# Kernel tuning notes

Hardware: AMD Instinct MI355X
Metric: run time of the kernel (lower is better)

The kernel has to match this reference:

```python
import jax, jax.numpy as jnp
import numpy as np
from jax import lax

MAX_OBJ = 100
IOU_THRES = 0.45
SCORE_THRES = 0.25
MAX_WH = 7680.0

# xywh -> xyxy conversion matrix (same as ONNX_ORT.convert_matrix)
CONVERT = jnp.array([[1, 0, 1, 0],
                     [0, 1, 0, 1],
                     [-0.5, 0, 0.5, 0],
                     [0, -0.5, 0, 0.5]], dtype=jnp.float32)


def _iou_one_vs_all(box, boxes):
    # box: [4] xyxy, boxes: [N,4] xyxy
    x1 = jnp.maximum(box[0], boxes[:, 0])
    y1 = jnp.maximum(box[1], boxes[:, 1])
    x2 = jnp.minimum(box[2], boxes[:, 2])
    y2 = jnp.minimum(box[3], boxes[:, 3])
    inter = jnp.clip(x2 - x1, 0.0) * jnp.clip(y2 - y1, 0.0)
    a = (box[2] - box[0]) * (box[3] - box[1])
    b = (boxes[:, 2] - boxes[:, 0]) * (boxes[:, 3] - boxes[:, 1])
    return inter / (a + b - inter + 1e-9)


def _nms_indices(nmsbox, max_score):
    # Greedy class-offset NMS; returns [MAX_OBJ] indices, -1 for padding.
    valid0 = max_score >= SCORE_THRES

    def step(valid, _):
        s = jnp.where(valid, max_score, -1.0)
        i = jnp.argmax(s)
        ok = s[i] >= SCORE_THRES
        iou = _iou_one_vs_all(nmsbox[i], nmsbox)
        valid = valid & (iou <= IOU_THRES)
        valid = valid.at[i].set(False)
        return valid, jnp.where(ok, i, -1)

    _, idxs = lax.scan(step, valid0, None, length=MAX_OBJ)
    return idxs


def _forward(x1, x2, num_labels1, num_labels2):
    B, N1, _ = x1.shape
    N2 = x2.shape[1]
    # pad x1 class scores with zeros for model2's labels (appended at end)
    x1p = jnp.concatenate([x1, jnp.zeros((B, N1, num_labels2), x1.dtype)], axis=2)
    # pad x2: insert zeros for model1's labels between conf and its own classes
    x2p = jnp.concatenate([x2[:, :, 0:5],
                           jnp.zeros((B, N2, num_labels1), x2.dtype),
                           x2[:, :, 5:]], axis=2)
    x = jnp.concatenate([x1p, x2p], axis=1)  # [B, N1+N2, 5+C1+C2]

    boxes = x[:, :, :4] @ CONVERT            # xywh -> xyxy, [B,N,4]
    conf = x[:, :, 4:5]
    scores = x[:, :, 5:] * conf              # [B,N,C]
    max_score = scores.max(axis=2)           # [B,N]
    cat_id = scores.argmax(axis=2)           # [B,N]
    # class-offset boxes so NMS is class-aware
    nmsbox = boxes + cat_id[..., None].astype(boxes.dtype) * MAX_WH

    idxs = jax.vmap(_nms_indices)(lax.stop_gradient(nmsbox),
                                  lax.stop_gradient(max_score))  # [B,MAX_OBJ]
    mask = idxs >= 0
    si = jnp.maximum(idxs, 0)
    sel_boxes = jnp.take_along_axis(boxes, si[..., None], axis=1)      # [B,MAX_OBJ,4]
    sel_cat = jnp.take_along_axis(cat_id, si, axis=1).astype(boxes.dtype)
    sel_score = jnp.take_along_axis(max_score, si, axis=1)

    mf = mask.astype(boxes.dtype)
    Xcol = jnp.where(mask, jnp.arange(B)[:, None], -1).astype(boxes.dtype)
    out = jnp.concatenate([Xcol[..., None],
                           sel_boxes * mf[..., None],
                           (sel_cat * mf)[..., None],
                           (sel_score * mf)[..., None]], axis=2)
    return out.reshape(B * MAX_OBJ, 7)


def setup_inputs() -> dict:
    key = jax.random.key(0)
    k1, k2 = jax.random.split(key)
    x1 = jax.random.uniform(k1, (4, 25200, 85), dtype=jnp.float32)
    x2 = jax.random.uniform(k2, (4, 25200, 25), dtype=jnp.float32)
    return {"x1": x1, "x2": x2, "num_labels1": 80, "num_labels2": 20}


def reference(x1, x2, num_labels1, num_labels2):
    return _forward(x1, x2, num_labels1, num_labels2)
```

## Files before the change

kernel.cpp:

```cpp
#include <hip/hip_runtime.h>
#include <stdint.h>

#pragma clang fp contract(off)

#define BATCH 4
#define N1 25200
#define NROW 50400
#define NCLS 100
#define TOT (BATCH*NROW)
#define CAPB 1280
#define SCORE_T 0.25f
#define IOU_T 0.45f
#define MAXWH 7680.0f

#define X1_SLAB 64
#define X1_SPB 394
#define X2_SLAB 256
#define X2_SPB 99

#define BIN_SLICES 128
#define BIN_SL 394

typedef unsigned long long u64;

__device__ __forceinline__ u64 pack_key(unsigned sb, int n, int cid) {
    return ((u64)sb << 32) | ((u64)(unsigned)((n ^ 0xFFFF) & 0xFFFF) << 8) | (u64)(unsigned)cid;
}

__device__ __forceinline__ bool sup_test(float inter, float sum) {
    float d = (sum - inter) + 1e-9f;
    float t1 = IOU_T * d;
    bool hi = inter > t1 * 1.00001f;
    bool lo = inter < t1 * 0.99999f;
    if (__builtin_expect(!(hi || lo), 0)) return (inter / d) > IOU_T;
    return hi;
}

__device__ __forceinline__ float rl(float v, int srcLane) {
    return __int_as_float(__builtin_amdgcn_readlane(__float_as_int(v), srcLane));
}

__device__ __forceinline__ void blk2bucket(int blk, int& b, int& c) {
    if (blk < BATCH * 20) { b = blk / 20; c = 80 + (blk - b * 20); }
    else { int z = blk - BATCH * 20; b = z / 80; c = z - b * 80; }
}

__device__ __forceinline__ int prefix_ge(const u64* list, int cnt, u64 T) {
    int lo = 0, hi = cnt;
    while (lo < hi) {
        int mid = (lo + hi) >> 1;
        if (list[mid] >= T) lo = mid + 1; else hi = mid;
    }
    return lo;
}

__device__ __forceinline__ void sort_desc(u64* sk, int L, int t) {
    bool act = (t * 8) < L;
    u64 r[8];
    if (act) {
#pragma unroll
        for (int e = 0; e < 8; ++e) r[e] = sk[t * 8 + e];
    }
    for (int k = 2; k <= L; k <<= 1) {
        for (int j = k >> 1; j > 0; j >>= 1) {
            if (j >= 512) {
                if (act) {
#pragma unroll
                    for (int e = 0; e < 8; ++e) sk[t * 8 + e] = r[e];
                }
                __syncthreads();
                if (act) {
                    bool iAmLo = (t & (j >> 3)) == 0;
                    bool descSeg = (t & (k >> 3)) == 0;
                    bool takeMax = (descSeg == iAmLo);
#pragma unroll
                    for (int e = 0; e < 8; ++e) {
                        u64 u = r[e];
                        u64 v = sk[(t * 8 + e) ^ j];
                        bool uGE = (u >= v);
                        r[e] = (takeMax == uGE) ? u : v;
                    }
                }
                __syncthreads();
            } else if (j >= 8) {
                if (act) {
                    int dt = j >> 3;
                    bool iAmLo = (t & dt) == 0;
                    bool descSeg = (t & (k >> 3)) == 0;
                    bool takeMax = (descSeg == iAmLo);
#pragma unroll
                    for (int e = 0; e < 8; ++e) {
                        u64 u = r[e];
                        u64 v = __shfl_xor(u, dt, 64);
                        bool uGE = (u >= v);
                        r[e] = (takeMax == uGE) ? u : v;
                    }
                }
            } else {
                if (act) {
#pragma unroll
                    for (int e = 0; e < 8; ++e) {
                        if (!(e & j)) {
                            int e2 = e | j;
                            bool descSeg = (k >= 8) ? ((t & (k >> 3)) == 0)
                                                    : ((e & k) == 0);
                            u64 lo = r[e], hi = r[e2];
                            bool sw = descSeg ? (lo < hi) : (lo > hi);
                            if (sw) { r[e] = hi; r[e2] = lo; }
                        }
                    }
                }
            }
        }
    }
    if (act) {
#pragma unroll
        for (int e = 0; e < 8; ++e) sk[t * 8 + e] = r[e];
    }
    __syncthreads();
}

__global__ __launch_bounds__(256) void k_rows(const float* __restrict__ x1,
                                              const float* __restrict__ x2,
                                              float4* __restrict__ boxes4,
                                              u64* __restrict__ rowKey) {
    __shared__ float4 ld4[1600];
    float* ld = (float*)ld4;
    int blk = blockIdx.x;
    int t = threadIdx.x;
    const int NX1 = BATCH * X1_SPB;
    if (blk < NX1) {
        int b = blk / X1_SPB, s = blk - b * X1_SPB;
        int r0 = s * X1_SLAB;
        int nr = min(X1_SLAB, N1 - r0);
        const float4* src = (const float4*)(x1 + ((size_t)b * N1 + r0) * 85);
        int count4 = (nr * 85) >> 2;
        for (int i = t; i < count4; i += 256) ld4[i] = src[i];
        __syncthreads();
        int row = t >> 2, sub = t & 3;
        if (row < nr) {
            const float* p = ld + row * 85;
            float conf = p[4];
            u64 key = 0ULL;
            int base = sub * 20;
            for (int c = 0; c < 20; ++c) {
                int j = base + c;
                float v = p[5 + j] * conf;
                u64 kk = ((u64)__float_as_uint(v) << 32) | (unsigned)~(unsigned)j;
                if (kk > key) key = kk;
            }
            u64 o;
            o = __shfl_xor(key, 1, 64); if (o > key) key = o;
            o = __shfl_xor(key, 2, 64); if (o > key) key = o;
            if (sub == 0) {
                float best = __uint_as_float((unsigned)(key >> 32));
                int bestj = ~(unsigned)key;
                int n = r0 + row;
                int r = b * NROW + n;
                u64 outk = 0ULL;
                if (best >= SCORE_T) {
                    float cx = p[0], cy = p[1], w = p[2], h = p[3];
                    boxes4[r] = make_float4(cx - 0.5f * w, cy - 0.5f * h,
                                            cx + 0.5f * w, cy + 0.5f * h);
                    outk = pack_key((unsigned)(key >> 32), n, bestj);
                }
                rowKey[r] = outk;
            }
        }
    } else {
        int blk2 = blk - NX1;
        int b = blk2 / X2_SPB, s = blk2 - b * X2_SPB;
        int r0 = s * X2_SLAB;
        int nr = min(X2_SLAB, N1 - r0);
        const float4* src = (const float4*)(x2 + ((size_t)b * N1 + r0) * 25);
        int count4 = (nr * 25) >> 2;
        for (int i = t; i < count4; i += 256) ld4[i] = src[i];
        __syncthreads();
        if (t < nr) {
            const float* p = ld + t * 25;
            float conf = p[4];
            float best = 0.0f; int bestj = 0;
            for (int j2 = 0; j2 < 20; ++j2) {
                float v = p[5 + j2] * conf;
                if (v > best) { best = v; bestj = 80 + j2; }
            }
            int n = N1 + r0 + t;
            int r = b * NROW + n;
            u64 outk = 0ULL;
            if (best >= SCORE_T) {
                float cx = p[0], cy = p[1], w = p[2], h = p[3];
                boxes4[r] = make_float4(cx - 0.5f * w, cy - 0.5f * h,
                                        cx + 0.5f * w, cy + 0.5f * h);
                outk = pack_key(__float_as_uint(best), n, bestj);
            }
            rowKey[r] = outk;
        }
    }
}

__global__ __launch_bounds__(256) void k_bin(const u64* __restrict__ rowKey,
                                             u64* __restrict__ csrKey,
                                             int* __restrict__ fill) {
    __shared__ u64 keys[BIN_SL];
    __shared__ int cnt[NCLS];
    __shared__ int base[NCLS];
    __shared__ int cur[NCLS];
    int blk = blockIdx.x;
    int b = blk / BIN_SLICES, s = blk - b * BIN_SLICES;
    int r0 = s * BIN_SL;
    int nr = min(BIN_SL, NROW - r0);
    int t = threadIdx.x;
    if (t < NCLS) { cnt[t] = 0; cur[t] = 0; }
    __syncthreads();
    const u64* src = rowKey + (size_t)b * NROW + r0;
    for (int i = t; i < nr; i += 256) {
        u64 k = src[i];
        keys[i] = k;
        if (k != 0ULL) atomicAdd(&cnt[(int)(k & 0xFF)], 1);
    }
    __syncthreads();
    if (t < NCLS && cnt[t] > 0)
        base[t] = atomicAdd(&fill[b * NCLS + t], cnt[t]);
    __syncthreads();
    for (int i = t; i < nr; i += 256) {
        u64 k = keys[i];
        if (k != 0ULL) {
            int c = (int)(k & 0xFF);
            int p = base[c] + atomicAdd(&cur[c], 1);
            if (p < CAPB) csrKey[(size_t)(b * NCLS + c) * CAPB + p] = k;
        }
    }
}

__global__ __launch_bounds__(256) void k_nms(const float4* __restrict__ boxes4,
                                             const u64* __restrict__ csrKey,
                                             const int* __restrict__ fill,
                                             u64* __restrict__ accKey,
                                             int* __restrict__ accCnt) {
    __shared__ u64 sk[2048];
    __shared__ float4 cQ[CAPB];
    __shared__ float4 accQ[100];
    __shared__ float accA[100];
    int b, c; blk2bucket(blockIdx.x, b, c);
    int bucket = b * NCLS + c;
    int t = threadIdx.x;
    int lane = t & 63;
    int cnt0 = min(fill[bucket], CAPB);
    if (cnt0 == 0) { if (t == 0) accCnt[bucket] = 0; return; }
    const u64* src = csrKey + (size_t)bucket * CAPB;
    int L = 512; while (L < cnt0) L <<= 1;
    for (int i = t; i < L; i += 256) sk[i] = (i < cnt0) ? src[i] : 0ULL;
    __syncthreads();
    sort_desc(sk, L, t);
    float off = (float)c * MAXWH;
    for (int i = t; i < cnt0; i += 256) {
        u64 k = sk[i];
        int n = 0xFFFF ^ (int)((k >> 8) & 0xFFFF);
        float4 v = boxes4[b * NROW + n];
        v.x += off; v.y += off; v.z += off; v.w += off;
        cQ[i] = v;
    }
    __syncthreads();
    if (t >= 64) return;

    int m = 0;
    for (int base = 0; base < cnt0 && m < 100; base += 64) {
        int j = base + lane;
        bool alive = (j < cnt0);
        float4 a = make_float4(0.f, 0.f, 0.f, 0.f);
        float aA = 0.f; u64 myKey = 0ULL;
        if (alive) {
            myKey = sk[j];
            a = cQ[j];
            aA = (a.z - a.x) * (a.w - a.y);
        }
        int k2 = 0;
        while (k2 < m) {
            if (__ballot(alive) == 0ULL) break;
            int rem = m - k2;
            if (rem >= 8) {
#pragma unroll
                for (int u = 0; u < 8; ++u) {
                    float4 q = accQ[k2 + u];
                    float qa = accA[k2 + u];
                    float xx1 = fmaxf(a.x, q.x), yy1 = fmaxf(a.y, q.y);
                    float xx2 = fminf(a.z, q.z), yy2 = fminf(a.w, q.w);
                    float inter = fmaxf(xx2 - xx1, 0.f) * fmaxf(yy2 - yy1, 0.f);
                    alive = alive && !sup_test(inter, qa + aA);
                }
                k2 += 8;
            } else {
                for (int u = 0; u < rem; ++u) {
                    float4 q = accQ[k2 + u];
                    float qa = accA[k2 + u];
                    float xx1 = fmaxf(a.x, q.x), yy1 = fmaxf(a.y, q.y);
                    float xx2 = fminf(a.z, q.z), yy2 = fminf(a.w, q.w);
                    float inter = fmaxf(xx2 - xx1, 0.f) * fmaxf(yy2 - yy1, 0.f);
                    alive = alive && !sup_test(inter, qa + aA);
                }
                k2 = m;
            }
        }
        u64 av = __ballot(alive);
        int accIdx = -1;
        while (av != 0ULL && m < 100) {
            int f = __builtin_ctzll(av);
            float qx = rl(a.x, f), qy = rl(a.y, f);
            float qz = rl(a.z, f), qw = rl(a.w, f);
            if (lane == f) { accIdx = m; alive = false; }
            ++m;
            if (alive) {
                float qa = (qz - qx) * (qw - qy);
                float xx1 = fmaxf(a.x, qx), yy1 = fmaxf(a.y, qy);
                float xx2 = fminf(a.z, qz), yy2 = fminf(a.w, qw);
                float inter = fmaxf(xx2 - xx1, 0.f) * fmaxf(yy2 - yy1, 0.f);
                alive = !sup_test(inter, qa + aA);
            }
            av = __ballot(alive);
        }
        if (accIdx >= 0) {
            accQ[accIdx] = a; accA[accIdx] = aA;
            accKey[(size_t)bucket * 100 + accIdx] = myKey;
        }
    }
    if (lane == 0) accCnt[bucket] = m;
}

__global__ __launch_bounds__(256) void k_merge(const float4* __restrict__ boxes4,
                                               const u64* __restrict__ accKey,
                                               const int* __restrict__ accCnt,
                                               float* __restrict__ out) {
    __shared__ u64 sk[1024];
    __shared__ u64 head[NCLS];
    __shared__ int cnts[NCLS];
    __shared__ int pc[NCLS];
    int b = blockIdx.x, t = threadIdx.x;
    const u64* base = accKey + (size_t)b * NCLS * 100;
    if (t < NCLS) {
        int cc = accCnt[b * NCLS + t];
        cnts[t] = cc;
        head[t] = (cc > 0) ? base[t * 100] : 0ULL;
    }
    __syncthreads();
    int S = 0, ne = 0; u64 mn = ~0ULL;
    for (int c = 0; c < NCLS; ++c) {
        int cc = cnts[c];
        S += cc;
        if (cc > 0) { ++ne; u64 h = head[c]; if (h < mn) mn = h; }
    }
    u64 T;
    bool bisect;
    if (S <= 900)            { T = 0ULL; bisect = false; }
    else if (ne == NCLS)     { T = mn;   bisect = false; }
    else                     { T = 0ULL; bisect = true;  }
    if (t < NCLS) pc[t] = bisect ? 0 : prefix_ge(base + t * 100, cnts[t], T);
    __syncthreads();
    int G = 0;
    for (int c = 0; c < NCLS; ++c) G += pc[c];
    if (G > 1000) bisect = true;
    if (bisect) {
        u64 lo = 0ULL, hi = ~0ULL;
        for (int it = 0; it < 64; ++it) {
            u64 mid = lo + ((hi - lo) >> 1);
            if (t < NCLS) pc[t] = prefix_ge(base + t * 100, cnts[t], mid);
            __syncthreads();
            int cnt = 0;
            for (int c = 0; c < NCLS; ++c) cnt += pc[c];
            if (cnt >= 100 && cnt <= 1000) { T = mid; G = cnt; break; }
            if (cnt < 100) hi = mid; else lo = mid;
            __syncthreads();
        }
    }
    if (t < NCLS) {
        int off = 0;
        for (int c = 0; c < t; ++c) off += pc[c];
        int p = pc[t];
        for (int j = 0; j < p; ++j) sk[off + j] = base[t * 100 + j];
    }
    for (int i = G + t; i < 1024; i += 256) sk[i] = 0ULL;
    __syncthreads();
    sort_desc(sk, 1024, t);
    if (t < 100) {
        u64 k = sk[t];
        float* o7 = out + (size_t)(b * 100 + t) * 7;
        if (k == 0ULL) {
            o7[0] = -1.0f;
            o7[1] = 0.0f; o7[2] = 0.0f; o7[3] = 0.0f;
            o7[4] = 0.0f; o7[5] = 0.0f; o7[6] = 0.0f;
        } else {
            int n = 0xFFFF ^ (int)((k >> 8) & 0xFFFF);
            int cid = (int)(k & 0xFF);
            float4 bx = boxes4[b * NROW + n];
            o7[0] = (float)b;
            o7[1] = bx.x; o7[2] = bx.y; o7[3] = bx.z; o7[4] = bx.w;
            o7[5] = (float)cid;
            o7[6] = __uint_as_float((unsigned)(k >> 32));
        }
    }
}

extern "C" void kernel_launch(void* const* d_in, const int* in_sizes, int n_in,
                              void* d_out, int out_size, void* d_ws, size_t ws_size,
                              hipStream_t stream) {
    const float* x1 = (const float*)d_in[0];
    const float* x2 = (const float*)d_in[1];
    float* out = (float*)d_out;

    float4* boxes4 = (float4*)d_ws;
    u64* rowKey = (u64*)(boxes4 + TOT);
    u64* csrKey = rowKey + TOT;
    u64* accKey = csrKey + (size_t)BATCH * NCLS * CAPB;
    int* fill   = (int*)(accKey + (size_t)BATCH * NCLS * 100);
    int* accCnt = fill + BATCH * NCLS;

    hipMemsetAsync(fill, 0, sizeof(int) * BATCH * NCLS, stream);

    int rowBlocks = BATCH * X1_SPB + BATCH * X2_SPB;
    k_rows<<<rowBlocks, 256, 0, stream>>>(x1, x2, boxes4, rowKey);
    k_bin<<<BATCH * BIN_SLICES, 256, 0, stream>>>(rowKey, csrKey, fill);
    k_nms<<<BATCH * NCLS, 256, 0, stream>>>(boxes4, csrKey, fill, accKey, accCnt);
    k_merge<<<BATCH, 256, 0, stream>>>(boxes4, accKey, accCnt, out);
}
```

Before: 134.3 us.

## Parallelize per-class NMS suppression across four wavefronts per block

The NMS kernel previously ran the greedy suppression on a single wavefront, leaving the other three idle. Now all four wavefronts test a 256-candidate group against the already accepted boxes in parallel and publish alive masks through shared memory. Wavefront 0 then sequentially resolves the survivors against boxes accepted within the group. This adds two block barriers per group and some redundant recomputation in exchange for more parallel IoU work.

Measured after the change: 134.5 us. No clear change (+0.1%).

```diff
diff --git a/kernel.cpp b/kernel.cpp
--- a/kernel.cpp
+++ b/kernel.cpp
@@ -241,10 +241,12 @@
     __shared__ float4 cQ[CAPB];
     __shared__ float4 accQ[100];
     __shared__ float accA[100];
+    __shared__ u64 aliveMask[4];
+    __shared__ int mSh;
     int b, c; blk2bucket(blockIdx.x, b, c);
     int bucket = b * NCLS + c;
     int t = threadIdx.x;
-    int lane = t & 63;
+    int lane = t & 63, wid = t >> 6;
     int cnt0 = min(fill[bucket], CAPB);
     if (cnt0 == 0) { if (t == 0) accCnt[bucket] = 0; return; }
     const u64* src = csrKey + (size_t)bucket * CAPB;
@@ -260,70 +262,116 @@
         v.x += off; v.y += off; v.z += off; v.w += off;
         cQ[i] = v;
     }
-    __syncthreads();
-    if (t >= 64) return;
-
-    int m = 0;
-    for (int base = 0; base < cnt0 && m < 100; base += 64) {
-        int j = base + lane;
-        bool alive = (j < cnt0);
-        float4 a = make_float4(0.f, 0.f, 0.f, 0.f);
-        float aA = 0.f; u64 myKey = 0ULL;
-        if (alive) {
-            myKey = sk[j];
-            a = cQ[j];
-            aA = (a.z - a.x) * (a.w - a.y);
-        }
-        int k2 = 0;
-        while (k2 < m) {
-            if (__ballot(alive) == 0ULL) break;
-            int rem = m - k2;
-            if (rem >= 8) {
-#pragma unroll
-                for (int u = 0; u < 8; ++u) {
-                    float4 q = accQ[k2 + u];
-                    float qa = accA[k2 + u];
-                    float xx1 = fmaxf(a.x, q.x), yy1 = fmaxf(a.y, q.y);
-                    float xx2 = fminf(a.z, q.z), yy2 = fminf(a.w, q.w);
-                    float inter = fmaxf(xx2 - xx1, 0.f) * fmaxf(yy2 - yy1, 0.f);
-                    alive = alive && !sup_test(inter, qa + aA);
-                }
-                k2 += 8;
-            } else {
-                for (int u = 0; u < rem; ++u) {
-                    float4 q = accQ[k2 + u];
-                    float qa = accA[k2 + u];
-                    float xx1 = fmaxf(a.x, q.x), yy1 = fmaxf(a.y, q.y);
-                    float xx2 = fminf(a.z, q.z), yy2 = fminf(a.w, q.w);
-                    float inter = fmaxf(xx2 - xx1, 0.f) * fmaxf(yy2 - yy1, 0.f);
-                    alive = alive && !sup_test(inter, qa + aA);
-                }
-                k2 = m;
-            }
-        }
-        u64 av = __ballot(alive);
-        int accIdx = -1;
-        while (av != 0ULL && m < 100) {
-            int f = __builtin_ctzll(av);
-            float qx = rl(a.x, f), qy = rl(a.y, f);
-            float qz = rl(a.z, f), qw = rl(a.w, f);
-            if (lane == f) { accIdx = m; alive = false; }
-            ++m;
-            if (alive) {
-                float qa = (qz - qx) * (qw - qy);
-                float xx1 = fmaxf(a.x, qx), yy1 = fmaxf(a.y, qy);
-                float xx2 = fminf(a.z, qz), yy2 = fminf(a.w, qw);
-                float inter = fmaxf(xx2 - xx1, 0.f) * fmaxf(yy2 - yy1, 0.f);
-                alive = !sup_test(inter, qa + aA);
-            }
-            av = __ballot(alive);
-        }
-        if (accIdx >= 0) {
-            accQ[accIdx] = a; accA[accIdx] = aA;
-            accKey[(size_t)bucket * 100 + accIdx] = myKey;
-        }
-    }
-    if (lane == 0) accCnt[bucket] = m;
+    if (t == 0) mSh = 0;
+    __syncthreads();
+
+    int nG = (cnt0 + 255) >> 8;
+    for (int g = 0; g < nG; ++g) {
+        int mSnap = mSh;
+        if (mSnap < 100) {
+            int j = ((g << 2) + wid) * 64 + lane;
+            bool alive = (j < cnt0);
+            float4 a = make_float4(0.f, 0.f, 0.f, 0.f);
+            float aA = 0.f;
+            if (alive) { a = cQ[j]; aA = (a.z - a.x) * (a.w - a.y); }
+            int k2 = 0;
+            while (k2 < mSnap) {
+                if (__ballot(alive) == 0ULL) break;
+                int rem = mSnap - k2;
+                if (rem >= 8) {
+#pragma unroll
+                    for (int u = 0; u < 8; ++u) {
+                        float4 q = accQ[k2 + u];
+                        float qa = accA[k2 + u];
+                        float xx1 = fmaxf(a.x, q.x), yy1 = fmaxf(a.y, q.y);
+                        float xx2 = fminf(a.z, q.z), yy2 = fminf(a.w, q.w);
+                        float inter = fmaxf(xx2 - xx1, 0.f) * fmaxf(yy2 - yy1, 0.f);
+                        alive = alive && !sup_test(inter, qa + aA);
+                    }
+                    k2 += 8;
+                } else {
+                    for (int u = 0; u < rem; ++u) {
+                        float4 q = accQ[k2 + u];
+                        float qa = accA[k2 + u];
+                        float xx1 = fmaxf(a.x, q.x), yy1 = fmaxf(a.y, q.y);
+                        float xx2 = fminf(a.z, q.z), yy2 = fminf(a.w, q.w);
+                        float inter = fmaxf(xx2 - xx1, 0.f) * fmaxf(yy2 - yy1, 0.f);
+                        alive = alive && !sup_test(inter, qa + aA);
+                    }
+                    k2 = mSnap;
+                }
+            }
+            u64 wmask = __ballot(alive);
+            if (lane == 0) aliveMask[wid] = wmask;
+        }
+        __syncthreads();
+        if (mSnap < 100 && wid == 0) {
+            int mNow = mSnap;
+            for (int s = 0; s < 4 && mNow < 100; ++s) {
+                int j = ((g << 2) + s) * 64 + lane;
+                bool alive = ((aliveMask[s] >> lane) & 1ULL) && (j < cnt0);
+                float4 a = make_float4(0.f, 0.f, 0.f, 0.f);
+                float aA = 0.f; u64 myKey = 0ULL;
+                if (alive) {
+                    a = cQ[j];
+                    aA = (a.z - a.x) * (a.w - a.y);
+                    myKey = sk[j];
+                }
+                int k2 = mSnap;
+                while (k2 < mNow) {
+                    if (__ballot(alive) == 0ULL) break;
+                    int rem = mNow - k2;
+                    if (rem >= 8) {
+#pragma unroll
+                        for (int u = 0; u < 8; ++u) {
+                            float4 q = accQ[k2 + u];
+                            float qa = accA[k2 + u];
+                            float xx1 = fmaxf(a.x, q.x), yy1 = fmaxf(a.y, q.y);
+                            float xx2 = fminf(a.z, q.z), yy2 = fminf(a.w, q.w);
+                            float inter = fmaxf(xx2 - xx1, 0.f) * fmaxf(yy2 - yy1, 0.f);
+                            alive = alive && !sup_test(inter, qa + aA);
+                        }
+                        k2 += 8;
+                    } else {
+                        for (int u = 0; u < rem; ++u) {
+                            float4 q = accQ[k2 + u];
+                            float qa = accA[k2 + u];
+                            float xx1 = fmaxf(a.x, q.x), yy1 = fmaxf(a.y, q.y);
+                            float xx2 = fminf(a.z, q.z), yy2 = fminf(a.w, q.w);
+                            float inter = fmaxf(xx2 - xx1, 0.f) * fmaxf(yy2 - yy1, 0.f);
+                            alive = alive && !sup_test(inter, qa + aA);
+                        }
+                        k2 = mNow;
+                    }
+                }
+                u64 av = __ballot(alive);
+                int accIdx = -1;
+                while (av != 0ULL && mNow < 100) {
+                    int f = __builtin_ctzll(av);
+                    float qx = rl(a.x, f), qy = rl(a.y, f);
+                    float qz = rl(a.z, f), qw = rl(a.w, f);
+                    if (lane == f) { accIdx = mNow; alive = false; }
+                    ++mNow;
+                    if (alive) {
+                        float qa = (qz - qx) * (qw - qy);
+                        float xx1 = fmaxf(a.x, qx), yy1 = fmaxf(a.y, qy);
+                        float xx2 = fminf(a.z, qz), yy2 = fminf(a.w, qw);
+                        float inter = fmaxf(xx2 - xx1, 0.f) * fmaxf(yy2 - yy1, 0.f);
+                        alive = !sup_test(inter, qa + aA);
+                    }
+                    av = __ballot(alive);
+                }
+                if (accIdx >= 0) {
+                    accQ[accIdx] = a;
+                    accA[accIdx] = aA;
+                    accKey[(size_t)bucket * 100 + accIdx] = myKey;
+                }
+            }
+            if (lane == 0) mSh = mNow;
+        }
+        __syncthreads();
+    }
+    if (t == 0) accCnt[bucket] = mSh;
 }
 
 __global__ __launch_bounds__(256) void k_merge(const float4* __restrict__ boxes4,
```

## Parallelize per-class NMS across full block using suppression bitmask matrix

Applied to the files above, without the earlier changes.

The per-bucket NMS now uses all 256 threads instead of one wavefront. Each group of 256 candidates is first filtered against boxes already accepted. Every thread then computes a 256-bit suppression row against later candidates in its group, and wave 0 resolves the greedy selection by scanning those bitmasks. Accepted boxes are kept as indices into cQ rather than copied, so their areas are recomputed. This raises IoU work per group (full pairwise matrix) and adds block barriers, in exchange for less serial ballot/readlane work.

Result: slower. 167.5 us (+24.7%).

```diff
diff --git a/kernel.cpp b/kernel.cpp
--- a/kernel.cpp
+++ b/kernel.cpp
@@ -34,10 +34,6 @@
     bool lo = inter < t1 * 0.99999f;
     if (__builtin_expect(!(hi || lo), 0)) return (inter / d) > IOU_T;
     return hi;
-}
-
-__device__ __forceinline__ float rl(float v, int srcLane) {
-    return __int_as_float(__builtin_amdgcn_readlane(__float_as_int(v), srcLane));
 }
 
 __device__ __forceinline__ void blk2bucket(int blk, int& b, int& c) {
@@ -239,12 +235,14 @@
                                              int* __restrict__ accCnt) {
     __shared__ u64 sk[2048];
     __shared__ float4 cQ[CAPB];
-    __shared__ float4 accQ[100];
-    __shared__ float accA[100];
+    __shared__ u64 supMat[256][4];
+    __shared__ int accJ[100];
+    __shared__ u64 aliveM[4];
+    __shared__ int mSh;
     int b, c; blk2bucket(blockIdx.x, b, c);
     int bucket = b * NCLS + c;
     int t = threadIdx.x;
-    int lane = t & 63;
+    int lane = t & 63, wid = t >> 6;
     int cnt0 = min(fill[bucket], CAPB);
     if (cnt0 == 0) { if (t == 0) accCnt[bucket] = 0; return; }
     const u64* src = csrKey + (size_t)bucket * CAPB;
@@ -260,29 +258,28 @@
         v.x += off; v.y += off; v.z += off; v.w += off;
         cQ[i] = v;
     }
-    __syncthreads();
-    if (t >= 64) return;
-
-    int m = 0;
-    for (int base = 0; base < cnt0 && m < 100; base += 64) {
-        int j = base + lane;
-        bool alive = (j < cnt0);
+    if (t == 0) mSh = 0;
+    __syncthreads();
+
+    int nG = (cnt0 + 255) >> 8;
+    for (int g = 0; g < nG; ++g) {
+        int mSnap = mSh;
+        if (mSnap >= 100) break;
+        int gbase = g << 8;
+        int jmax = min(256, cnt0 - gbase);
+        bool alive = (t < jmax);
         float4 a = make_float4(0.f, 0.f, 0.f, 0.f);
-        float aA = 0.f; u64 myKey = 0ULL;
-        if (alive) {
-            myKey = sk[j];
-            a = cQ[j];
-            aA = (a.z - a.x) * (a.w - a.y);
-        }
+        float aA = 0.f;
+        if (alive) { a = cQ[gbase + t]; aA = (a.z - a.x) * (a.w - a.y); }
         int k2 = 0;
-        while (k2 < m) {
+        while (k2 < mSnap) {
             if (__ballot(alive) == 0ULL) break;
-            int rem = m - k2;
+            int rem = mSnap - k2;
             if (rem >= 8) {
 #pragma unroll
                 for (int u = 0; u < 8; ++u) {
-                    float4 q = accQ[k2 + u];
-                    float qa = accA[k2 + u];
+                    float4 q = cQ[accJ[k2 + u]];
+                    float qa = (q.z - q.x) * (q.w - q.y);
                     float xx1 = fmaxf(a.x, q.x), yy1 = fmaxf(a.y, q.y);
                     float xx2 = fminf(a.z, q.z), yy2 = fminf(a.w, q.w);
                     float inter = fmaxf(xx2 - xx1, 0.f) * fmaxf(yy2 - yy1, 0.f);
@@ -291,39 +288,60 @@
                 k2 += 8;
             } else {
                 for (int u = 0; u < rem; ++u) {
-                    float4 q = accQ[k2 + u];
-                    float qa = accA[k2 + u];
+                    float4 q = cQ[accJ[k2 + u]];
+                    float qa = (q.z - q.x) * (q.w - q.y);
                     float xx1 = fmaxf(a.x, q.x), yy1 = fmaxf(a.y, q.y);
                     float xx2 = fminf(a.z, q.z), yy2 = fminf(a.w, q.w);
                     float inter = fmaxf(xx2 - xx1, 0.f) * fmaxf(yy2 - yy1, 0.f);
                     alive = alive && !sup_test(inter, qa + aA);
                 }
-                k2 = m;
-            }
-        }
-        u64 av = __ballot(alive);
-        int accIdx = -1;
-        while (av != 0ULL && m < 100) {
-            int f = __builtin_ctzll(av);
-            float qx = rl(a.x, f), qy = rl(a.y, f);
-            float qz = rl(a.z, f), qw = rl(a.w, f);
-            if (lane == f) { accIdx = m; alive = false; }
-            ++m;
-            if (alive) {
-                float qa = (qz - qx) * (qw - qy);
-                float xx1 = fmaxf(a.x, qx), yy1 = fmaxf(a.y, qy);
-                float xx2 = fminf(a.z, qz), yy2 = fminf(a.w, qw);
-                float inter = fmaxf(xx2 - xx1, 0.f) * fmaxf(yy2 - yy1, 0.f);
-                alive = !sup_test(inter, qa + aA);
-            }
-            av = __ballot(alive);
-        }
-        if (accIdx >= 0) {
-            accQ[accIdx] = a; accA[accIdx] = aA;
-            accKey[(size_t)bucket * 100 + accIdx] = myKey;
-        }
-    }
-    if (lane == 0) accCnt[bucket] = m;
+                k2 = mSnap;
+            }
+        }
+        u64 wmask = __ballot(alive);
+        if (lane == 0) aliveM[wid] = wmask;
+        u64 row0 = 0, row1 = 0, row2 = 0, row3 = 0;
+        for (int jj = 0; jj < jmax; ++jj) {
+            float4 q = cQ[gbase + jj];
+            float qa = (q.z - q.x) * (q.w - q.y);
+            float xx1 = fmaxf(a.x, q.x), yy1 = fmaxf(a.y, q.y);
+            float xx2 = fminf(a.z, q.z), yy2 = fminf(a.w, q.w);
+            float inter = fmaxf(xx2 - xx1, 0.f) * fmaxf(yy2 - yy1, 0.f);
+            bool sup = (jj > t) ? sup_test(inter, aA + qa) : (jj == t);
+            u64 bit = (u64)sup << (jj & 63);
+            if (jj < 64)        row0 |= bit;
+            else if (jj < 128)  row1 |= bit;
+            else if (jj < 192)  row2 |= bit;
+            else                row3 |= bit;
+        }
+        supMat[t][0] = row0; supMat[t][1] = row1;
+        supMat[t][2] = row2; supMat[t][3] = row3;
+        __syncthreads();
+        if (wid == 0) {
+            u64 rem0 = aliveM[0], rem1 = aliveM[1];
+            u64 rem2 = aliveM[2], rem3 = aliveM[3];
+            int m = mSnap;
+            while (m < 100) {
+                int f;
+                if (rem0)      f = __builtin_ctzll(rem0);
+                else if (rem1) f = 64 + __builtin_ctzll(rem1);
+                else if (rem2) f = 128 + __builtin_ctzll(rem2);
+                else if (rem3) f = 192 + __builtin_ctzll(rem3);
+                else break;
+                if (lane == 0) accJ[m] = gbase + f;
+                ++m;
+                u64 r0 = supMat[f][0], r1 = supMat[f][1];
+                u64 r2 = supMat[f][2], r3 = supMat[f][3];
+                rem0 &= ~r0; rem1 &= ~r1; rem2 &= ~r2; rem3 &= ~r3;
+            }
+            if (lane == 0) mSh = m;
+        }
+        __syncthreads();
+    }
+    int mF = mSh;
+    for (int i = t; i < mF; i += 256)
+        accKey[(size_t)bucket * 100 + i] = sk[accJ[i]];
+    if (t == 0) accCnt[bucket] = mF;
 }
 
 __global__ __launch_bounds__(256) void k_merge(const float4* __restrict__ boxes4,
```

## Split per-class NMS into separate sort and single-wave greedy kernels

Applied to the files above, without the earlier changes.

The fused per-class NMS kernel becomes two kernels. A 256-thread sort kernel sorts each bucket's keys in shared memory and writes them back in place. A 64-thread greedy kernel then runs the suppression loop, loading keys from global memory and gathering boxes lazily only for the chunks it actually visits. The goal is to free the three idle waves and the large shared-memory footprint that the greedy phase used to hold, which should raise occupancy and skip gathering boxes past the point where 100 are kept. In exchange it adds a kernel launch, a global round trip for the sorted keys, and uncached global gathers inside the greedy loop.

Result: slower. 137.4 us (+2.3%).

```diff
diff --git a/kernel.cpp b/kernel.cpp
--- a/kernel.cpp
+++ b/kernel.cpp
@@ -232,37 +232,37 @@
     }
 }
 
-__global__ __launch_bounds__(256) void k_nms(const float4* __restrict__ boxes4,
-                                             const u64* __restrict__ csrKey,
-                                             const int* __restrict__ fill,
-                                             u64* __restrict__ accKey,
-                                             int* __restrict__ accCnt) {
+__global__ __launch_bounds__(256) void k_sort(u64* __restrict__ csrKey,
+                                              const int* __restrict__ fill,
+                                              int* __restrict__ accCnt) {
     __shared__ u64 sk[2048];
-    __shared__ float4 cQ[CAPB];
+    int b, c; blk2bucket(blockIdx.x, b, c);
+    int bucket = b * NCLS + c;
+    int t = threadIdx.x;
+    int cnt0 = min(fill[bucket], CAPB);
+    if (cnt0 == 0) { if (t == 0) accCnt[bucket] = 0; return; }
+    u64* src = csrKey + (size_t)bucket * CAPB;
+    int L = 512; while (L < cnt0) L <<= 1;
+    for (int i = t; i < L; i += 256) sk[i] = (i < cnt0) ? src[i] : 0ULL;
+    __syncthreads();
+    sort_desc(sk, L, t);
+    for (int i = t; i < cnt0; i += 256) src[i] = sk[i];
+}
+
+__global__ __launch_bounds__(64) void k_greedy(const float4* __restrict__ boxes4,
+                                               const u64* __restrict__ csrKey,
+                                               const int* __restrict__ fill,
+                                               u64* __restrict__ accKey,
+                                               int* __restrict__ accCnt) {
     __shared__ float4 accQ[100];
     __shared__ float accA[100];
     int b, c; blk2bucket(blockIdx.x, b, c);
     int bucket = b * NCLS + c;
-    int t = threadIdx.x;
-    int lane = t & 63;
+    int lane = threadIdx.x;
     int cnt0 = min(fill[bucket], CAPB);
-    if (cnt0 == 0) { if (t == 0) accCnt[bucket] = 0; return; }
-    const u64* src = csrKey + (size_t)bucket * CAPB;
-    int L = 512; while (L < cnt0) L <<= 1;
-    for (int i = t; i < L; i += 256) sk[i] = (i < cnt0) ? src[i] : 0ULL;
-    __syncthreads();
-    sort_desc(sk, L, t);
+    if (cnt0 == 0) { if (lane == 0) accCnt[bucket] = 0; return; }
+    const u64* skB = csrKey + (size_t)bucket * CAPB;
     float off = (float)c * MAXWH;
-    for (int i = t; i < cnt0; i += 256) {
-        u64 k = sk[i];
-        int n = 0xFFFF ^ (int)((k >> 8) & 0xFFFF);
-        float4 v = boxes4[b * NROW + n];
-        v.x += off; v.y += off; v.z += off; v.w += off;
-        cQ[i] = v;
-    }
-    __syncthreads();
-    if (t >= 64) return;
-
     int m = 0;
     for (int base = 0; base < cnt0 && m < 100; base += 64) {
         int j = base + lane;
@@ -270,8 +270,10 @@
         float4 a = make_float4(0.f, 0.f, 0.f, 0.f);
         float aA = 0.f; u64 myKey = 0ULL;
         if (alive) {
-            myKey = sk[j];
-            a = cQ[j];
+            myKey = skB[j];
+            int n = 0xFFFF ^ (int)((myKey >> 8) & 0xFFFF);
+            a = boxes4[b * NROW + n];
+            a.x += off; a.y += off; a.z += off; a.w += off;
             aA = (a.z - a.x) * (a.w - a.y);
         }
         int k2 = 0;
@@ -418,6 +420,7 @@
     int rowBlocks = BATCH * X1_SPB + BATCH * X2_SPB;
     k_rows<<<rowBlocks, 256, 0, stream>>>(x1, x2, boxes4, rowKey);
     k_bin<<<BATCH * BIN_SLICES, 256, 0, stream>>>(rowKey, csrKey, fill);
-    k_nms<<<BATCH * NCLS, 256, 0, stream>>>(boxes4, csrKey, fill, accKey, accCnt);
+    k_sort<<<BATCH * NCLS, 256, 0, stream>>>(csrKey, fill, accCnt);
+    k_greedy<<<BATCH * NCLS, 64, 0, stream>>>(boxes4, csrKey, fill, accKey, accCnt);
     k_merge<<<BATCH, 256, 0, stream>>>(boxes4, accKey, accCnt, out);
 }
```
